# Kernel tuning notes

Measured on AMD Instinct MI355X. Metric: run time of the kernel, lower is better.

The kernel has to match this reference:

```python
import jax, jax.numpy as jnp
import numpy as np

D_MODEL = 32
HEADS = 4
DK = D_MODEL // HEADS


def _linear(x, W, b):
    # torch nn.Linear: y = x @ W.T + b, W has shape (out, in)
    return jnp.einsum('...i,oi->...o', x, W) + b


def setup_inputs() -> dict:
    key = jax.random.key(0)
    ks = jax.random.split(key, 11)
    B, T, C, H, W = 4, 8, 3, 256, 256
    s_in = 1.0 / np.sqrt(C)
    s_d = 1.0 / np.sqrt(D_MODEL)
    return {
        'z_receive': jax.random.normal(ks[0], (B, T, C, H, W), dtype=jnp.float32),
        'W_in': jax.random.uniform(ks[1], (D_MODEL, C), jnp.float32, -s_in, s_in),
        'b_in': jax.random.uniform(ks[2], (D_MODEL,), jnp.float32, -s_in, s_in),
        'W_q': jax.random.uniform(ks[3], (D_MODEL, D_MODEL), jnp.float32, -s_d, s_d),
        'b_q': jax.random.uniform(ks[4], (D_MODEL,), jnp.float32, -s_d, s_d),
        'W_k': jax.random.uniform(ks[5], (D_MODEL, D_MODEL), jnp.float32, -s_d, s_d),
        'b_k': jax.random.uniform(ks[6], (D_MODEL,), jnp.float32, -s_d, s_d),
        'W_v': jax.random.uniform(ks[7], (D_MODEL, D_MODEL), jnp.float32, -s_d, s_d),
        'b_v': jax.random.uniform(ks[8], (D_MODEL,), jnp.float32, -s_d, s_d),
        'W_o': jax.random.uniform(ks[9], (3, D_MODEL), jnp.float32, -s_d, s_d),
        'b_o': jax.random.uniform(ks[10], (3,), jnp.float32, -s_d, s_d),
    }


def reference(z_receive, W_in, b_in, W_q, b_q, W_k, b_k, W_v, b_v, W_o, b_o):
    B, T, C, H, W = z_receive.shape
    # (B,T,3,H,W) -> (B,H,W,T,3): per-pixel temporal sequences
    x = jnp.transpose(z_receive, (0, 3, 4, 1, 2))
    x = _linear(x, W_in, b_in)            # (B,H,W,T,d_model)
    q = _linear(x, W_q, b_q)
    k = _linear(x, W_k, b_k)
    v = _linear(x, W_v, b_v)

    def split_heads(t):
        return t.reshape(B, H, W, T, HEADS, DK)  # (B,H,W,T,h,dk)

    q_h, k_h, v_h = split_heads(q), split_heads(k), split_heads(v)
    scale = 1.0 / np.sqrt(DK)
    # attention over temporal axis per pixel per head: (B,H,W,h,Tq,Tk)
    attn = jnp.einsum('bxytnd,bxysnd->bxynts', q_h, k_h) * scale
    w = jax.nn.softmax(attn, axis=-1)
    out = jnp.einsum('bxynts,bxysnd->bxytnd', w, v_h)  # (B,H,W,T,h,dk)
    out = out.reshape(B, H, W, T, HEADS * DK)
    out_last = out[:, :, :, -1, :]                      # (B,H,W,d_model)
    z_fuse = _linear(out_last, W_o, b_o)                # (B,H,W,3)
    return jnp.transpose(z_fuse, (0, 3, 1, 2))          # (B,3,H,W)
```

## Files before the change

### kernel.cpp

```cpp
#include <hip/hip_runtime.h>
#include <math.h>

constexpr int TT = 8;
constexpr int CC = 3;
constexpr int DM = 32;
constexpr int NH = 4;
constexpr int HW = 256 * 256;


__global__ __launch_bounds__(256) void attn_fused(
    const float* __restrict__ z,
    const float* __restrict__ W_in, const float* __restrict__ b_in,
    const float* __restrict__ W_q,  const float* __restrict__ b_q,
    const float* __restrict__ W_k,  const float* __restrict__ b_k,
    const float* __restrict__ W_v,  const float* __restrict__ b_v,
    const float* __restrict__ W_o,  const float* __restrict__ b_o,
    float* __restrict__ out)
{
    __shared__ float sQW[DM][CC], sKW[DM][CC];
    __shared__ float sqb0[DM], skb0[DM];
    __shared__ float sWoV[CC][NH][DM];
    __shared__ float sbv2[DM];
    __shared__ float sM[NH][CC][CC], sA[NH][CC], sN[NH][CC], sB0[NH];
    __shared__ float sG[CC][NH][CC], syb2[CC];

    const int tid = threadIdx.x;

    if (tid < 96) {
        int o = tid / 3, c = tid % 3;
        float a = 0.f;
        #pragma unroll
        for (int i = 0; i < DM; ++i) a += W_q[o*DM+i] * W_in[i*CC+c];
        sQW[o][c] = a;
    } else if (tid < 192) {
        int t = tid - 96, o = t / 3, c = t % 3;
        float a = 0.f;
        #pragma unroll
        for (int i = 0; i < DM; ++i) a += W_k[o*DM+i] * W_in[i*CC+c];
        sKW[o][c] = a;
    } else if (tid < 224) {
        int o = tid - 192;
        float a = b_q[o];
        #pragma unroll
        for (int i = 0; i < DM; ++i) a += W_q[o*DM+i] * b_in[i];
        sqb0[o] = a;
    } else {
        int o = tid - 224;
        float a = b_k[o];
        #pragma unroll
        for (int i = 0; i < DM; ++i) a += W_k[o*DM+i] * b_in[i];
        skb0[o] = a;
    }
    for (int e = tid; e < CC*NH*DM + DM; e += 256) {
        if (e < CC*NH*DM) {
            int c = e >> 7, n = (e >> 5) & 3, i = e & 31;
            float a = 0.f;
            #pragma unroll
            for (int j = 0; j < 8; ++j)
                a += W_o[c*DM + n*8 + j] * W_v[(n*8+j)*DM + i];
            sWoV[c][n][i] = a;
        } else {
            int o = e - CC*NH*DM;
            float a = b_v[o];
            #pragma unroll
            for (int i = 0; i < DM; ++i) a += W_v[o*DM+i] * b_in[i];
            sbv2[o] = a;
        }
    }
    __syncthreads();

    const float scale = 0.35355339059327373f;
    if (tid < 36) {
        int n = tid / 9, r = tid % 9, c = r / 3, c2 = r % 3;
        float a = 0.f;
        #pragma unroll
        for (int j = 0; j < 8; ++j) a += sQW[n*8+j][c2] * sKW[n*8+j][c];
        sM[n][c][c2] = scale * a;
    } else if (tid < 48) {
        int idx = tid - 36, n = idx / 3, c = idx % 3;
        float a = 0.f;
        #pragma unroll
        for (int j = 0; j < 8; ++j) a += sqb0[n*8+j] * sKW[n*8+j][c];
        sA[n][c] = scale * a;
    } else if (tid < 60) {
        int idx = tid - 48, n = idx / 3, c2 = idx % 3;
        float a = 0.f;
        #pragma unroll
        for (int j = 0; j < 8; ++j) a += sQW[n*8+j][c2] * skb0[n*8+j];
        sN[n][c2] = scale * a;
    } else if (tid < 64) {
        int n = tid - 60;
        float a = 0.f;
        #pragma unroll
        for (int j = 0; j < 8; ++j) a += sqb0[n*8+j] * skb0[n*8+j];
        sB0[n] = scale * a;
    } else if (tid < 100) {
        int idx = tid - 64, c = idx / 12, r = idx % 12, n = r / 3, c2 = r % 3;
        float a = 0.f;
        #pragma unroll
        for (int i = 0; i < DM; ++i) a += sWoV[c][n][i] * W_in[i*CC+c2];
        sG[c][n][c2] = a;
    } else if (tid < 103) {
        int c = tid - 100;
        float a = b_o[c];
        #pragma unroll
        for (int o = 0; o < DM; ++o) a += W_o[c*DM+o] * sbv2[o];
        syb2[c] = a;
    }
    __syncthreads();

    const int p  = blockIdx.x * 256 + tid;
    const int hw = p & (HW - 1);
    const int b  = p >> 16;
    const float* zb = z + (size_t)b * TT * CC * HW + hw;

    float zv[TT][CC];
    #pragma unroll
    for (int s = 0; s < TT; ++s)
        #pragma unroll
        for (int c = 0; c < CC; ++c)
            zv[s][c] = zb[(s*CC + c) * HW];

    float qw[NH][CC], qb[NH];
    #pragma unroll
    for (int n = 0; n < NH; ++n) {
        qb[n] = sB0[n] + sN[n][0]*zv[7][0] + sN[n][1]*zv[7][1] + sN[n][2]*zv[7][2];
        #pragma unroll
        for (int c = 0; c < CC; ++c)
            qw[n][c] = sA[n][c] + sM[n][c][0]*zv[7][0] + sM[n][c][1]*zv[7][1] + sM[n][c][2]*zv[7][2];
    }

    float wz[NH][CC];
    #pragma unroll
    for (int n = 0; n < NH; ++n) {
        float sc[TT];
        float m = -1e30f;
        #pragma unroll
        for (int s = 0; s < TT; ++s) {
            float v = qb[n] + qw[n][0]*zv[s][0] + qw[n][1]*zv[s][1] + qw[n][2]*zv[s][2];
            sc[s] = v;
            m = fmaxf(m, v);
        }
        float l = 0.f;
        #pragma unroll
        for (int s = 0; s < TT; ++s) { float e = __expf(sc[s] - m); sc[s] = e; l += e; }
        float inv = 1.f / l;
        #pragma unroll
        for (int c = 0; c < CC; ++c) {
            float a = 0.f;
            #pragma unroll
            for (int s = 0; s < TT; ++s) a += sc[s] * zv[s][c];
            wz[n][c] = a * inv;
        }
    }

    #pragma unroll
    for (int c = 0; c < CC; ++c) {
        float a = syb2[c];
        #pragma unroll
        for (int n = 0; n < NH; ++n)
            #pragma unroll
            for (int c2 = 0; c2 < CC; ++c2)
                a += sG[c][n][c2] * wz[n][c2];
        out[((size_t)b * CC + c) * HW + hw] = a;
    }
}

extern "C" void kernel_launch(void* const* d_in, const int* in_sizes, int n_in,
                              void* d_out, int out_size, void* d_ws, size_t ws_size,
                              hipStream_t stream) {
    const float* z    = (const float*)d_in[0];
    const float* W_in = (const float*)d_in[1];
    const float* b_in = (const float*)d_in[2];
    const float* W_q  = (const float*)d_in[3];
    const float* b_q  = (const float*)d_in[4];
    const float* W_k  = (const float*)d_in[5];
    const float* b_k  = (const float*)d_in[6];
    const float* W_v  = (const float*)d_in[7];
    const float* b_v  = (const float*)d_in[8];
    const float* W_o  = (const float*)d_in[9];
    const float* b_o  = (const float*)d_in[10];
    float* out = (float*)d_out;

    const int B = in_sizes[0] / (TT * CC * HW);
    const int npix = B * HW;
    const int blocks = npix / 256;

    attn_fused<<<blocks, 256, 0, stream>>>(
        z, W_in, b_in, W_q, b_q, W_k, b_k, W_v, b_v, W_o, b_o, out);
}
```

Baseline: 94.54 us.

## Process four pixels per thread with float4 loads and prefetch before setup

Each thread now handles four adjacent pixels, loading the input with float4 vector loads and writing the output with float4 stores. The global loads are issued before the per-block weight-folding prologue so their latency overlaps the setup. Because each block now covers four times as many pixels, the redundant per-block weight precomputation is amortised over more work. The cost is higher register pressure (96 floats of input held per thread) and a quarter as many blocks, which lowers parallelism.

```diff
diff --git a/kernel.cpp b/kernel.cpp
--- a/kernel.cpp
+++ b/kernel.cpp
@@ -6,6 +6,7 @@
 constexpr int DM = 32;
 constexpr int NH = 4;
 constexpr int HW = 256 * 256;
+constexpr int PX = 4;
 
 
 __global__ __launch_bounds__(256) void attn_fused(
@@ -26,6 +27,18 @@
 
     const int tid = threadIdx.x;
 
+    const int t   = blockIdx.x * 256 + tid;
+    const int b   = t >> 14;
+    const int hw4 = (t & 16383);
+    const float4* zb = (const float4*)(z + (size_t)b * TT * CC * HW) + hw4;
+
+    float4 zv[TT][CC];
+    #pragma unroll
+    for (int s = 0; s < TT; ++s)
+        #pragma unroll
+        for (int c = 0; c < CC; ++c)
+            zv[s][c] = zb[(s*CC + c) * (HW/4)];
+
     if (tid < 96) {
         int o = tid / 3, c = tid % 3;
         float a = 0.f;
@@ -33,7 +46,7 @@
         for (int i = 0; i < DM; ++i) a += W_q[o*DM+i] * W_in[i*CC+c];
         sQW[o][c] = a;
     } else if (tid < 192) {
-        int t = tid - 96, o = t / 3, c = t % 3;
+        int tt = tid - 96, o = tt / 3, c = tt % 3;
         float a = 0.f;
         #pragma unroll
         for (int i = 0; i < DM; ++i) a += W_k[o*DM+i] * W_in[i*CC+c];
@@ -109,60 +122,67 @@
     }
     __syncthreads();
 
-    const int p  = blockIdx.x * 256 + tid;
-    const int hw = p & (HW - 1);
-    const int b  = p >> 16;
-    const float* zb = z + (size_t)b * TT * CC * HW + hw;
-
-    float zv[TT][CC];
+    float y[CC][PX];
+
     #pragma unroll
-    for (int s = 0; s < TT; ++s)
-        #pragma unroll
-        for (int c = 0; c < CC; ++c)
-            zv[s][c] = zb[(s*CC + c) * HW];
-
-    float qw[NH][CC], qb[NH];
-    #pragma unroll
-    for (int n = 0; n < NH; ++n) {
-        qb[n] = sB0[n] + sN[n][0]*zv[7][0] + sN[n][1]*zv[7][1] + sN[n][2]*zv[7][2];
-        #pragma unroll
-        for (int c = 0; c < CC; ++c)
-            qw[n][c] = sA[n][c] + sM[n][c][0]*zv[7][0] + sM[n][c][1]*zv[7][1] + sM[n][c][2]*zv[7][2];
-    }
-
-    float wz[NH][CC];
-    #pragma unroll
-    for (int n = 0; n < NH; ++n) {
-        float sc[TT];
-        float m = -1e30f;
-        #pragma unroll
-        for (int s = 0; s < TT; ++s) {
-            float v = qb[n] + qw[n][0]*zv[s][0] + qw[n][1]*zv[s][1] + qw[n][2]*zv[s][2];
-            sc[s] = v;
-            m = fmaxf(m, v);
-        }
-        float l = 0.f;
-        #pragma unroll
-        for (int s = 0; s < TT; ++s) { float e = __expf(sc[s] - m); sc[s] = e; l += e; }
-        float inv = 1.f / l;
+    for (int px = 0; px < PX; ++px) {
+        float zp[TT][CC];
+        #pragma unroll
+        for (int s = 0; s < TT; ++s)
+            #pragma unroll
+            for (int c = 0; c < CC; ++c)
+                zp[s][c] = ((const float*)&zv[s][c])[px];
+
+        float qw[NH][CC], qb[NH];
+        #pragma unroll
+        for (int n = 0; n < NH; ++n) {
+            qb[n] = sB0[n] + sN[n][0]*zp[7][0] + sN[n][1]*zp[7][1] + sN[n][2]*zp[7][2];
+            #pragma unroll
+            for (int c = 0; c < CC; ++c)
+                qw[n][c] = sA[n][c] + sM[n][c][0]*zp[7][0] + sM[n][c][1]*zp[7][1] + sM[n][c][2]*zp[7][2];
+        }
+
+        float wz[NH][CC];
+        #pragma unroll
+        for (int n = 0; n < NH; ++n) {
+            float sc[TT];
+            float m = -1e30f;
+            #pragma unroll
+            for (int s = 0; s < TT; ++s) {
+                float v = qb[n] + qw[n][0]*zp[s][0] + qw[n][1]*zp[s][1] + qw[n][2]*zp[s][2];
+                sc[s] = v;
+                m = fmaxf(m, v);
+            }
+            float l = 0.f;
+            #pragma unroll
+            for (int s = 0; s < TT; ++s) { float e = __expf(sc[s] - m); sc[s] = e; l += e; }
+            float inv = 1.f / l;
+            #pragma unroll
+            for (int c = 0; c < CC; ++c) {
+                float a = 0.f;
+                #pragma unroll
+                for (int s = 0; s < TT; ++s) a += sc[s] * zp[s][c];
+                wz[n][c] = a * inv;
+            }
+        }
+
         #pragma unroll
         for (int c = 0; c < CC; ++c) {
-            float a = 0.f;
-            #pragma unroll
-            for (int s = 0; s < TT; ++s) a += sc[s] * zv[s][c];
-            wz[n][c] = a * inv;
-        }
-    }
-
+            float a = syb2[c];
+            #pragma unroll
+            for (int n = 0; n < NH; ++n)
+                #pragma unroll
+                for (int c2 = 0; c2 < CC; ++c2)
+                    a += sG[c][n][c2] * wz[n][c2];
+            y[c][px] = a;
+        }
+    }
+
+    float4* ob = (float4*)(out + (size_t)b * CC * HW) + hw4;
     #pragma unroll
     for (int c = 0; c < CC; ++c) {
-        float a = syb2[c];
-        #pragma unroll
-        for (int n = 0; n < NH; ++n)
-            #pragma unroll
-            for (int c2 = 0; c2 < CC; ++c2)
-                a += sG[c][n][c2] * wz[n][c2];
-        out[((size_t)b * CC + c) * HW + hw] = a;
+        float4 v = make_float4(y[c][0], y[c][1], y[c][2], y[c][3]);
+        ob[c * (HW/4)] = v;
     }
 }
 
@@ -183,8 +203,8 @@
     float* out = (float*)d_out;
 
     const int B = in_sizes[0] / (TT * CC * HW);
-    const int npix = B * HW;
-    const int blocks = npix / 256;
+    const int nthreads = B * HW / PX;
+    const int blocks = nthreads / 256;
 
     attn_fused<<<blocks, 256, 0, stream>>>(
         z, W_in, b_in, W_q, b_q, W_k, b_k, W_v, b_v, W_o, b_o, out);
```

Result: slower. 100.7 us (+6.5%).
